# Performance work log

Measured on AMD Instinct MI355X. Metric: run time of the kernel, lower is better.

The kernel has to match this reference:

```python
import jax, jax.numpy as jnp
import numpy as np

D_MODEL = 1024
NUM_HEADS = 16
D_K = D_MODEL // NUM_HEADS
B, S = 2, 2048
NEG = -1e9


def setup_inputs() -> dict:
    key = jax.random.key(0)
    ks = jax.random.split(key, 12)
    scale = 1.0 / np.sqrt(D_MODEL)
    inp = {
        'q': jax.random.normal(ks[0], (B, S, D_MODEL), jnp.float32),
        'k': jax.random.normal(ks[1], (B, S, D_MODEL), jnp.float32),
        'v': jax.random.normal(ks[2], (B, S, D_MODEL), jnp.float32),
        'mask': jax.random.randint(ks[3], (1, 1, S, S), 0, 2, jnp.int32),
        'wq_w': jax.random.normal(ks[4], (D_MODEL, D_MODEL), jnp.float32) * scale,
        'wq_b': jnp.zeros((D_MODEL,), jnp.float32),
        'wk_w': jax.random.normal(ks[5], (D_MODEL, D_MODEL), jnp.float32) * scale,
        'wk_b': jnp.zeros((D_MODEL,), jnp.float32),
        'wv_w': jax.random.normal(ks[6], (D_MODEL, D_MODEL), jnp.float32) * scale,
        'wv_b': jnp.zeros((D_MODEL,), jnp.float32),
        'wo_w': jax.random.normal(ks[7], (D_MODEL, D_MODEL), jnp.float32) * scale,
        'wo_b': jnp.zeros((D_MODEL,), jnp.float32),
    }
    return inp


def _split_heads(x):
    # [B,S,D] -> [B,H,S,d_k]
    b, s, _ = x.shape
    return x.reshape(b, s, NUM_HEADS, D_K).transpose(0, 2, 1, 3)


def reference(q, k, v, mask, wq_w, wq_b, wk_w, wk_b, wv_w, wv_b, wo_w, wo_b):
    # torch Linear: y = x @ W.T + b
    qh = _split_heads(q @ wq_w.T + wq_b)
    kh = _split_heads(k @ wk_w.T + wk_b)
    vh = _split_heads(v @ wv_w.T + wv_b)
    scores = jnp.einsum('bhqd,bhkd->bhqk', qh, kh) / jnp.sqrt(jnp.float32(D_K))
    scores = jnp.where(mask == 0, jnp.float32(NEG), scores)
    attn = jax.nn.softmax(scores, axis=-1)  # dropout p=0 (eval): no-op
    x = jnp.einsum('bhqk,bhkd->bhqd', attn, vh)
    x = x.transpose(0, 2, 1, 3).reshape(q.shape[0], q.shape[1], D_MODEL)
    return x @ wo_w.T + wo_b
```

## Files before the change

### kernel.cpp

```cpp
#include <hip/hip_runtime.h>
#include <hip/hip_bf16.h>
#include <stdint.h>

#define S_LEN  2048
#define DMODEL 1024
#define NHEADS 16
#define DKH    64
#define KDIM   1024

typedef __bf16 bf16x8 __attribute__((ext_vector_type(8)));
typedef __bf16 bf16x2 __attribute__((ext_vector_type(2)));
typedef float  floatx4 __attribute__((ext_vector_type(4)));
typedef float  floatx16 __attribute__((ext_vector_type(16)));
typedef unsigned short ushort8v __attribute__((ext_vector_type(8)));
typedef unsigned int  uint32x2 __attribute__((ext_vector_type(2)));
typedef unsigned int  uint32x4 __attribute__((ext_vector_type(4)));

__device__ inline void gll16(const __bf16* g, const __bf16* l) {
    __builtin_amdgcn_global_load_lds(
        (const __attribute__((address_space(1))) void*)g,
        (__attribute__((address_space(3))) void*)l, 16, 0, 0);
}

__device__ inline float fast_exp2(float x) {
#if __has_builtin(__builtin_amdgcn_exp2f)
    return __builtin_amdgcn_exp2f(x);
#else
    return exp2f(x);
#endif
}

__device__ inline int bit_sign(uint32_t v, int idx) {
#if __has_builtin(__builtin_amdgcn_sbfe)
    return __builtin_amdgcn_sbfe((int)v, (uint32_t)idx, 1u);
#else
    return ((int)(v << (31 - idx))) >> 31;
#endif
}

__device__ inline void plswap(uint32_t& a, uint32_t& b) {
    asm volatile("v_permlane32_swap_b32 %0, %1" : "+v"(a), "+v"(b));
}

__global__ __launch_bounds__(256) void prep_kernel(
    const float* __restrict__ q, const float* __restrict__ k, const float* __restrict__ v,
    const float* __restrict__ wq, const float* __restrict__ wk, const float* __restrict__ wv,
    const float* __restrict__ wo, __bf16* __restrict__ out,
    const int* __restrict__ M, uint64_t* __restrict__ P) {
    if (blockIdx.x < 8192) {
        const size_t i8 = ((size_t)blockIdx.x * 256 + threadIdx.x) * 8;
        const float* src;
        if (i8 < 4194304u)        src = q  + i8;
        else if (i8 < 8388608u)   src = k  + (i8 - 4194304u);
        else if (i8 < 12582912u)  src = v  + (i8 - 8388608u);
        else if (i8 < 13631488u)  src = wq + (i8 - 12582912u);
        else if (i8 < 14680064u)  src = wk + (i8 - 13631488u);
        else if (i8 < 15728640u)  src = wv + (i8 - 14680064u);
        else                      src = wo + (i8 - 15728640u);
        floatx4 a = *(const floatx4*)src;
        floatx4 b = *(const floatx4*)(src + 4);
        bf16x8 r;
#pragma unroll
        for (int i = 0; i < 4; ++i) { r[i] = (__bf16)a[i]; r[i + 4] = (__bf16)b[i]; }
        *(bf16x8*)(out + i8) = r;
    } else {
        const size_t i = ((size_t)(blockIdx.x - 8192)) * 256 + threadIdx.x;
        uint64_t bits = __ballot(M[i] != 0);
        if ((threadIdx.x & 63) == 0) P[i >> 6] = bits;
    }
}

__global__ __launch_bounds__(256, 5) void qkv_gemm(
    const __bf16* __restrict__ qb, const __bf16* __restrict__ kb, const __bf16* __restrict__ vb,
    const __bf16* __restrict__ wqw, const __bf16* __restrict__ wkw, const __bf16* __restrict__ wvw,
    const float* __restrict__ biasq, const float* __restrict__ biask, const float* __restrict__ biasv,
    __bf16* __restrict__ qh, __bf16* __restrict__ kh, __bf16* __restrict__ vt) {
    __shared__ __align__(16) __bf16 As[2 * 128 * 32];
    __shared__ __align__(16) __bf16 Bs[2 * 64 * 32];

    const int lane = threadIdx.x & 63;
    const int wave = threadIdx.x >> 6;
    const int quad = lane >> 4;
    const int l15  = lane & 15;

    const int bid = blockIdx.x;
    const int job = bid >> 9;
    const int tt  = bid & 511;
    const __bf16* A; const __bf16* Bm; const float* bias; __bf16* C;
    int bx, by, MODE;
    if (job == 0)      { A = qb;  Bm = wqw; bias = biasq; C = qh; bx = tt & 15; by = tt >> 4; MODE = 0; }
    else if (job == 1) { A = kb;  Bm = wkw; bias = biask; C = kh; bx = tt & 15; by = tt >> 4; MODE = 0; }
    else               { A = wvw; Bm = vb;  bias = biasv; C = vt; bx = tt & 63; by = tt >> 6; MODE = 1; }

    const int m_t = by * 128, n_t = bx * 64;
    const int m0w = (wave >> 1) * 64, n0w = (wave & 1) * 32;

    const int lrow = lane >> 2;
    const int scol = ((lane & 3) ^ (lrow & 3)) * 8;

    floatx4 acc[4][2];
#pragma unroll
    for (int i = 0; i < 4; ++i)
#pragma unroll
        for (int j = 0; j < 2; ++j)
            acc[i][j] = (floatx4){0.f, 0.f, 0.f, 0.f};

    for (int kk = 0; kk < KDIM; kk += 64) {
#pragma unroll
        for (int u = 0; u < 6; ++u) {
            const int pi = wave * 6 + u;
            if (pi < 16) {
                const int panel = pi >> 3, rb = pi & 7;
                gll16(A + (size_t)(m_t + rb * 16 + lrow) * KDIM + kk + panel * 32 + scol,
                      As + (panel * 128 + rb * 16) * 32);
            } else {
                const int qi = pi - 16, panel = qi >> 2, rb = qi & 3;
                gll16(Bm + (size_t)(n_t + rb * 16 + lrow) * KDIM + kk + panel * 32 + scol,
                      Bs + (panel * 64 + rb * 16) * 32);
            }
        }
        __syncthreads();
        const int cq = (quad ^ (l15 & 3)) * 8;
#pragma unroll
        for (int p = 0; p < 2; ++p) {
            bf16x8 af[4], bfr[2];
#pragma unroll
            for (int i = 0; i < 4; ++i)
                af[i] = *(const bf16x8*)(As + (p * 128 + m0w + i * 16 + l15) * 32 + cq);
#pragma unroll
            for (int j = 0; j < 2; ++j)
                bfr[j] = *(const bf16x8*)(Bs + (p * 64 + n0w + j * 16 + l15) * 32 + cq);
#pragma unroll
            for (int i = 0; i < 4; ++i)
#pragma unroll
                for (int j = 0; j < 2; ++j)
                    acc[i][j] = __builtin_amdgcn_mfma_f32_16x16x32_bf16(af[i], bfr[j], acc[i][j], 0, 0, 0);
        }
        __syncthreads();
    }

#pragma unroll
    for (int j = 0; j < 2; ++j) {
        const int n = n_t + n0w + j * 16 + l15;
        float bn = (MODE == 1) ? 0.f : bias[n];
#pragma unroll
        for (int i = 0; i < 4; ++i) {
#pragma unroll
            for (int r = 0; r < 4; ++r) {
                const int m = m_t + m0w + i * 16 + quad * 4 + r;
                float bv = (MODE == 1) ? bias[m] : bn;
                float v = acc[i][j][r] + bv;
                size_t off;
                if (MODE == 0) {
                    off = ((size_t)((m >> 11) * 16 + (n >> 6)) * 2048 + (m & 2047)) * 64 + (n & 63);
                } else {
                    off = ((size_t)((n >> 11) * 16 + (m >> 6)) * 64 + (m & 63)) * 2048 + (n & 2047);
                }
                C[off] = (__bf16)v;
            }
        }
    }
}

__global__ __launch_bounds__(256) void gemm_out(const __bf16* __restrict__ A,
                                                const __bf16* __restrict__ Bm,
                                                const float* __restrict__ bias,
                                                float* __restrict__ C) {
    __shared__ __align__(16) __bf16 As[2 * 128 * 32];
    __shared__ __align__(16) __bf16 Bs[2 * 64 * 32];

    const int lane = threadIdx.x & 63;
    const int wave = threadIdx.x >> 6;
    const int quad = lane >> 4;
    const int l15  = lane & 15;
    const int m_t = blockIdx.y * 128, n_t = blockIdx.x * 64;
    const int m0w = (wave >> 1) * 64, n0w = (wave & 1) * 32;

    const int lrow = lane >> 2;
    const int scol = ((lane & 3) ^ (lrow & 3)) * 8;

    floatx4 acc[4][2];
#pragma unroll
    for (int i = 0; i < 4; ++i)
#pragma unroll
        for (int j = 0; j < 2; ++j)
            acc[i][j] = (floatx4){0.f, 0.f, 0.f, 0.f};

    for (int kk = 0; kk < KDIM; kk += 64) {
#pragma unroll
        for (int u = 0; u < 6; ++u) {
            const int pi = wave * 6 + u;
            if (pi < 16) {
                const int panel = pi >> 3, rb = pi & 7;
                gll16(A + (size_t)(m_t + rb * 16 + lrow) * KDIM + kk + panel * 32 + scol,
                      As + (panel * 128 + rb * 16) * 32);
            } else {
                const int qi = pi - 16, panel = qi >> 2, rb = qi & 3;
                gll16(Bm + (size_t)(n_t + rb * 16 + lrow) * KDIM + kk + panel * 32 + scol,
                      Bs + (panel * 64 + rb * 16) * 32);
            }
        }
        __syncthreads();
        const int cq = (quad ^ (l15 & 3)) * 8;
#pragma unroll
        for (int p = 0; p < 2; ++p) {
            bf16x8 af[4], bfr[2];
#pragma unroll
            for (int i = 0; i < 4; ++i)
                af[i] = *(const bf16x8*)(As + (p * 128 + m0w + i * 16 + l15) * 32 + cq);
#pragma unroll
            for (int j = 0; j < 2; ++j)
                bfr[j] = *(const bf16x8*)(Bs + (p * 64 + n0w + j * 16 + l15) * 32 + cq);
#pragma unroll
            for (int i = 0; i < 4; ++i)
#pragma unroll
                for (int j = 0; j < 2; ++j)
                    acc[i][j] = __builtin_amdgcn_mfma_f32_16x16x32_bf16(af[i], bfr[j], acc[i][j], 0, 0, 0);
        }
        __syncthreads();
    }

#pragma unroll
    for (int j = 0; j < 2; ++j) {
        const int n = n_t + n0w + j * 16 + l15;
        const float bn = bias[n];
#pragma unroll
        for (int i = 0; i < 4; ++i)
#pragma unroll
            for (int r = 0; r < 4; ++r) {
                const int m = m_t + m0w + i * 16 + quad * 4 + r;
                C[(size_t)m * 1024 + n] = acc[i][j][r] + bn;
            }
    }
}

__global__ __launch_bounds__(256, 4) void attn_kernel(const __bf16* __restrict__ Qh,
                                                      const __bf16* __restrict__ Kh,
                                                      const __bf16* __restrict__ Vt,
                                                      const uint64_t* __restrict__ PM,
                                                      __bf16* __restrict__ X) {
    __shared__ __align__(16) __bf16 Ks[2][4096];
    __shared__ __align__(16) __bf16 Vs[2][4096];

    const int lane = threadIdx.x & 63;
    const int wave = threadIdx.x >> 6;
    const int l31  = lane & 31;
    const int hi   = lane >> 5;
    const int kh   = wave & 1;
    const int qhf  = wave >> 1;

    const int bid  = blockIdx.x;
    const int xcd  = bid & 7;
    const int slot = bid >> 3;
    const int grp  = xcd * 4 + (slot >> 5);
    const int qt   = slot & 31;
    const int b = grp >> 4, h = grp & 15;
    const int qw = qt * 64 + qhf * 32;

    const __bf16* Qb = Qh + (size_t)(b * NHEADS + h) * S_LEN * DKH;
    const __bf16* Kb = Kh + (size_t)(b * NHEADS + h) * S_LEN * DKH;
    const __bf16* Vb = Vt + (size_t)(b * NHEADS + h) * DKH * S_LEN;
    const uint64_t* pr = PM + (size_t)(qw + l31) * (S_LEN / 64);

    const float cs = 0.18033688011112042f;

    uint32_t offK[2], offV[2];
#pragma unroll
    for (int i = 0; i < 2; ++i) {
        const int pi  = wave * 2 + i;
        const int khs = pi >> 2, kss = pi & 3;
        offK[i] = (uint32_t)((khs * 32 + l31) * DKH + kss * 16 + hi * 8);
        const int dts = pi >> 2, khv = (pi >> 1) & 1, cv = pi & 1;
        offV[i] = (uint32_t)((dts * 32 + l31) * S_LEN + khv * 32 + cv * 16 + hi * 8);
    }

    auto stage = [&](int p, int key0) {
#pragma unroll
        for (int i = 0; i < 2; ++i) {
            gll16(Kb + (size_t)key0 * DKH + offK[i], Ks[p] + (wave * 2 + i) * 512);
            gll16(Vb + (size_t)key0 + offV[i],       Vs[p] + (wave * 2 + i) * 512);
        }
    };

    bf16x8 qf[4];
#pragma unroll
    for (int ks = 0; ks < 4; ++ks)
        qf[ks] = *(const bf16x8*)(Qb + (size_t)(qw + l31) * DKH + ks * 16 + hi * 8);

    floatx16 o0, o1;
#pragma unroll
    for (int i = 0; i < 16; ++i) { o0[i] = 0.f; o1[i] = 0.f; }
    float ls0 = 0.f;

    const __bf16* Kl = &Ks[0][kh * 2048 + lane * 8];
    const __bf16* Vl = &Vs[0][kh * 1024 + lane * 8];

    stage(0, 0);
    uint64_t mwc = pr[0];

    for (int kt = 0; kt < 32; ++kt) {
        const int p = kt & 1;
        __syncthreads();
        if (kt < 31) stage(p ^ 1, (kt + 1) * 64);
        const uint64_t mw = mwc;
        if (kt < 31) mwc = pr[kt + 1];

        const __bf16* Kp = Kl + p * 4096;
        const __bf16* Vp = Vl + p * 4096;

        floatx16 st;
#pragma unroll
        for (int i = 0; i < 16; ++i) st[i] = 0.f;
#pragma unroll
        for (int ks = 0; ks < 4; ++ks) {
            bf16x8 kf = *(const bf16x8*)(Kp + ks * 512);
            st = __builtin_amdgcn_mfma_f32_32x32x16_bf16(kf, qf[ks], st, 0, 0, 0);
        }

        const uint32_t w32 = (uint32_t)(kh ? (mw >> 32) : mw);
        const uint32_t wsh = w32 >> (hi * 4);

        float e[16];
#pragma unroll
        for (int r = 0; r < 16; ++r) {
            const int cpos = (r & 3) + 8 * (r >> 2);
            float v = fast_exp2(st[r] * cs);
            const int sgn = bit_sign(wsh, cpos);
            e[r] = __builtin_bit_cast(float, __builtin_bit_cast(int, v) & sgn);
        }
        ls0 += (((e[0] + e[1]) + (e[2] + e[3])) + ((e[4] + e[5]) + (e[6] + e[7])))
             + (((e[8] + e[9]) + (e[10] + e[11])) + ((e[12] + e[13]) + (e[14] + e[15])));

        uint32_t w[8];
#pragma unroll
        for (int r2 = 0; r2 < 8; ++r2) {
            bf16x2 pp; pp[0] = (__bf16)e[2 * r2]; pp[1] = (__bf16)e[2 * r2 + 1];
            w[r2] = __builtin_bit_cast(uint32_t, pp);
        }
        plswap(w[0], w[2]);
        plswap(w[1], w[3]);
        plswap(w[4], w[6]);
        plswap(w[5], w[7]);
        uint32x4 f0 = {w[0], w[1], w[2], w[3]};
        uint32x4 f1 = {w[4], w[5], w[6], w[7]};
        bf16x8 pf0 = __builtin_bit_cast(bf16x8, f0);
        bf16x8 pf1 = __builtin_bit_cast(bf16x8, f1);

        bf16x8 vf;
        vf = *(const bf16x8*)(Vp + 0 * 2048 + 0 * 512);
        o0 = __builtin_amdgcn_mfma_f32_32x32x16_bf16(vf, pf0, o0, 0, 0, 0);
        vf = *(const bf16x8*)(Vp + 0 * 2048 + 1 * 512);
        o0 = __builtin_amdgcn_mfma_f32_32x32x16_bf16(vf, pf1, o0, 0, 0, 0);
        vf = *(const bf16x8*)(Vp + 1 * 2048 + 0 * 512);
        o1 = __builtin_amdgcn_mfma_f32_32x32x16_bf16(vf, pf0, o1, 0, 0, 0);
        vf = *(const bf16x8*)(Vp + 1 * 2048 + 1 * 512);
        o1 = __builtin_amdgcn_mfma_f32_32x32x16_bf16(vf, pf1, o1, 0, 0, 0);
    }

    float lsum2 = ls0 + __shfl_xor(ls0, 32);

    __syncthreads();
    float* red  = (float*)&Ks[0][0];
    float* redl = (float*)&Vs[0][0];
    if (kh == 1) {
#pragma unroll
        for (int g = 0; g < 16; ++g) red[(qhf * 32 + g) * 64 + lane] = o0[g];
#pragma unroll
        for (int g = 0; g < 16; ++g) red[(qhf * 32 + 16 + g) * 64 + lane] = o1[g];
        redl[qhf * 64 + lane] = lsum2;
    }
    __syncthreads();
    if (kh == 0) {
        const float lt  = lsum2 + redl[qhf * 64 + lane];
        const float inv = (lt > 0.f) ? (1.f / lt) : 0.f;
        unsigned short* xp = (unsigned short*)X +
            (size_t)(b * S_LEN + qw + l31) * DMODEL + h * DKH;
#pragma unroll
        for (int g = 0; g < 4; ++g) {
            float va = (o0[g * 4 + 0] + red[(qhf * 32 + g * 4 + 0) * 64 + lane]) * inv;
            float vb = (o0[g * 4 + 1] + red[(qhf * 32 + g * 4 + 1) * 64 + lane]) * inv;
            float vc = (o0[g * 4 + 2] + red[(qhf * 32 + g * 4 + 2) * 64 + lane]) * inv;
            float vd = (o0[g * 4 + 3] + red[(qhf * 32 + g * 4 + 3) * 64 + lane]) * inv;
            bf16x2 pa; pa[0] = (__bf16)va; pa[1] = (__bf16)vb;
            bf16x2 pb; pb[0] = (__bf16)vc; pb[1] = (__bf16)vd;
            uint32x2 wv = {__builtin_bit_cast(uint32_t, pa), __builtin_bit_cast(uint32_t, pb)};
            *(uint32x2*)(xp + g * 8 + hi * 4) = wv;
        }
#pragma unroll
        for (int g = 0; g < 4; ++g) {
            float va = (o1[g * 4 + 0] + red[(qhf * 32 + 16 + g * 4 + 0) * 64 + lane]) * inv;
            float vb = (o1[g * 4 + 1] + red[(qhf * 32 + 16 + g * 4 + 1) * 64 + lane]) * inv;
            float vc = (o1[g * 4 + 2] + red[(qhf * 32 + 16 + g * 4 + 2) * 64 + lane]) * inv;
            float vd = (o1[g * 4 + 3] + red[(qhf * 32 + 16 + g * 4 + 3) * 64 + lane]) * inv;
            bf16x2 pa; pa[0] = (__bf16)va; pa[1] = (__bf16)vb;
            bf16x2 pb; pb[0] = (__bf16)vc; pb[1] = (__bf16)vd;
            uint32x2 wv = {__builtin_bit_cast(uint32_t, pa), __builtin_bit_cast(uint32_t, pb)};
            *(uint32x2*)(xp + 32 + g * 8 + hi * 4) = wv;
        }
    }
}

extern "C" void kernel_launch(void* const* d_in, const int* in_sizes, int n_in,
                              void* d_out, int out_size, void* d_ws, size_t ws_size,
                              hipStream_t stream) {
    const float* q   = (const float*)d_in[0];
    const float* k   = (const float*)d_in[1];
    const float* v   = (const float*)d_in[2];
    const int*   msk = (const int*)d_in[3];
    const float* wq  = (const float*)d_in[4];
    const float* wqb = (const float*)d_in[5];
    const float* wk  = (const float*)d_in[6];
    const float* wkb = (const float*)d_in[7];
    const float* wv  = (const float*)d_in[8];
    const float* wvb = (const float*)d_in[9];
    const float* wo  = (const float*)d_in[10];
    const float* wob = (const float*)d_in[11];

    char* ws = (char*)d_ws;
    __bf16*   qh   = (__bf16*)(ws);
    __bf16*   kh   = (__bf16*)(ws + 8388608);
    __bf16*   vt   = (__bf16*)(ws + 16777216);
    uint64_t* pm   = (uint64_t*)(ws + 25165824);
    __bf16*   cb   = (__bf16*)(ws + 25690112);
    __bf16*   qb   = cb;
    __bf16*   kb   = cb + 4194304;
    __bf16*   vb   = cb + 8388608;
    __bf16*   wqbf = cb + 12582912;
    __bf16*   wkbf = cb + 13631488;
    __bf16*   wvbf = cb + 14680064;
    __bf16*   wobf = cb + 15728640;
    __bf16*   xa   = qb;

    prep_kernel<<<24576, 256, 0, stream>>>(q, k, v, wq, wk, wv, wo, cb, msk, pm);
    qkv_gemm<<<1536, 256, 0, stream>>>(qb, kb, vb, wqbf, wkbf, wvbf, wqb, wkb, wvb, qh, kh, vt);
    attn_kernel<<<1024, 256, 0, stream>>>(qh, kh, vt, pm, xa);
    gemm_out<<<dim3(16, 32), 256, 0, stream>>>(xa, wobf, wob, (float*)d_out);
}
```

Before: 285.8 us.

## Load K/V fragments directly from global to registers, drop LDS staging

Replaces the double-buffered LDS staging of K and V tiles with direct per-wave global loads into registers. K fragments are prefetched one tile ahead and the loop is unrolled by two. This removes the per-iteration block barrier and LDS traffic but exposes global load latency and raises register use. The permlane32 swap also uses the compiler builtin when available.

```diff
diff --git a/kernel.cpp b/kernel.cpp
--- a/kernel.cpp
+++ b/kernel.cpp
@@ -39,7 +39,13 @@
 }
 
 __device__ inline void plswap(uint32_t& a, uint32_t& b) {
+#if __has_builtin(__builtin_amdgcn_permlane32_swap)
+    auto r = __builtin_amdgcn_permlane32_swap((int)a, (int)b, false, false);
+    a = (uint32_t)r[0];
+    b = (uint32_t)r[1];
+#else
     asm volatile("v_permlane32_swap_b32 %0, %1" : "+v"(a), "+v"(b));
+#endif
 }
 
 __global__ __launch_bounds__(256) void prep_kernel(
@@ -239,8 +245,8 @@
                                                       const __bf16* __restrict__ Vt,
                                                       const uint64_t* __restrict__ PM,
                                                       __bf16* __restrict__ X) {
-    __shared__ __align__(16) __bf16 Ks[2][4096];
-    __shared__ __align__(16) __bf16 Vs[2][4096];
+    __shared__ __align__(16) float red[64 * 64];
+    __shared__ float redl[128];
 
     const int lane = threadIdx.x & 63;
     const int wave = threadIdx.x >> 6;
@@ -264,23 +270,9 @@
 
     const float cs = 0.18033688011112042f;
 
-    uint32_t offK[2], offV[2];
-#pragma unroll
-    for (int i = 0; i < 2; ++i) {
-        const int pi  = wave * 2 + i;
-        const int khs = pi >> 2, kss = pi & 3;
-        offK[i] = (uint32_t)((khs * 32 + l31) * DKH + kss * 16 + hi * 8);
-        const int dts = pi >> 2, khv = (pi >> 1) & 1, cv = pi & 1;
-        offV[i] = (uint32_t)((dts * 32 + l31) * S_LEN + khv * 32 + cv * 16 + hi * 8);
-    }
-
-    auto stage = [&](int p, int key0) {
-#pragma unroll
-        for (int i = 0; i < 2; ++i) {
-            gll16(Kb + (size_t)key0 * DKH + offK[i], Ks[p] + (wave * 2 + i) * 512);
-            gll16(Vb + (size_t)key0 + offV[i],       Vs[p] + (wave * 2 + i) * 512);
-        }
-    };
+    const int kOff  = l31 * DKH + hi * 8;
+    const int vOff0 = l31 * S_LEN + hi * 8;
+    const int vOff1 = (32 + l31) * S_LEN + hi * 8;
 
     bf16x8 qf[4];
 #pragma unroll
@@ -292,30 +284,44 @@
     for (int i = 0; i < 16; ++i) { o0[i] = 0.f; o1[i] = 0.f; }
     float ls0 = 0.f;
 
-    const __bf16* Kl = &Ks[0][kh * 2048 + lane * 8];
-    const __bf16* Vl = &Vs[0][kh * 1024 + lane * 8];
-
-    stage(0, 0);
+    bf16x8 kf0, kf1, kf2, kf3;
+    {
+        const __bf16* kp = Kb + (size_t)(kh * 32) * DKH + kOff;
+        kf0 = *(const bf16x8*)(kp);
+        kf1 = *(const bf16x8*)(kp + 16);
+        kf2 = *(const bf16x8*)(kp + 32);
+        kf3 = *(const bf16x8*)(kp + 48);
+    }
     uint64_t mwc = pr[0];
 
+#pragma unroll 2
     for (int kt = 0; kt < 32; ++kt) {
-        const int p = kt & 1;
-        __syncthreads();
-        if (kt < 31) stage(p ^ 1, (kt + 1) * 64);
+        const int kb0 = kt * 64 + kh * 32;
+
+        const __bf16* vp0 = Vb + (size_t)kb0 + vOff0;
+        const __bf16* vp1 = Vb + (size_t)kb0 + vOff1;
+        bf16x8 vf0 = *(const bf16x8*)(vp0);
+        bf16x8 vf1 = *(const bf16x8*)(vp0 + 16);
+        bf16x8 vf2 = *(const bf16x8*)(vp1);
+        bf16x8 vf3 = *(const bf16x8*)(vp1 + 16);
+
+        floatx16 st;
+#pragma unroll
+        for (int i = 0; i < 16; ++i) st[i] = 0.f;
+        st = __builtin_amdgcn_mfma_f32_32x32x16_bf16(kf0, qf[0], st, 0, 0, 0);
+        st = __builtin_amdgcn_mfma_f32_32x32x16_bf16(kf1, qf[1], st, 0, 0, 0);
+        st = __builtin_amdgcn_mfma_f32_32x32x16_bf16(kf2, qf[2], st, 0, 0, 0);
+        st = __builtin_amdgcn_mfma_f32_32x32x16_bf16(kf3, qf[3], st, 0, 0, 0);
+
+        if (kt < 31) {
+            const __bf16* kp = Kb + (size_t)(kb0 + 64) * DKH + kOff;
+            kf0 = *(const bf16x8*)(kp);
+            kf1 = *(const bf16x8*)(kp + 16);
+            kf2 = *(const bf16x8*)(kp + 32);
+            kf3 = *(const bf16x8*)(kp + 48);
+        }
         const uint64_t mw = mwc;
         if (kt < 31) mwc = pr[kt + 1];
-
-        const __bf16* Kp = Kl + p * 4096;
-        const __bf16* Vp = Vl + p * 4096;
-
-        floatx16 st;
-#pragma unroll
-        for (int i = 0; i < 16; ++i) st[i] = 0.f;
-#pragma unroll
-        for (int ks = 0; ks < 4; ++ks) {
-            bf16x8 kf = *(const bf16x8*)(Kp + ks * 512);
-            st = __builtin_amdgcn_mfma_f32_32x32x16_bf16(kf, qf[ks], st, 0, 0, 0);
-        }
 
         const uint32_t w32 = (uint32_t)(kh ? (mw >> 32) : mw);
         const uint32_t wsh = w32 >> (hi * 4);
@@ -346,22 +352,14 @@
         bf16x8 pf0 = __builtin_bit_cast(bf16x8, f0);
         bf16x8 pf1 = __builtin_bit_cast(bf16x8, f1);
 
-        bf16x8 vf;
-        vf = *(const bf16x8*)(Vp + 0 * 2048 + 0 * 512);
-        o0 = __builtin_amdgcn_mfma_f32_32x32x16_bf16(vf, pf0, o0, 0, 0, 0);
-        vf = *(const bf16x8*)(Vp + 0 * 2048 + 1 * 512);
-        o0 = __builtin_amdgcn_mfma_f32_32x32x16_bf16(vf, pf1, o0, 0, 0, 0);
-        vf = *(const bf16x8*)(Vp + 1 * 2048 + 0 * 512);
-        o1 = __builtin_amdgcn_mfma_f32_32x32x16_bf16(vf, pf0, o1, 0, 0, 0);
-        vf = *(const bf16x8*)(Vp + 1 * 2048 + 1 * 512);
-        o1 = __builtin_amdgcn_mfma_f32_32x32x16_bf16(vf, pf1, o1, 0, 0, 0);
+        o0 = __builtin_amdgcn_mfma_f32_32x32x16_bf16(vf0, pf0, o0, 0, 0, 0);
+        o0 = __builtin_amdgcn_mfma_f32_32x32x16_bf16(vf1, pf1, o0, 0, 0, 0);
+        o1 = __builtin_amdgcn_mfma_f32_32x32x16_bf16(vf2, pf0, o1, 0, 0, 0);
+        o1 = __builtin_amdgcn_mfma_f32_32x32x16_bf16(vf3, pf1, o1, 0, 0, 0);
     }
 
     float lsum2 = ls0 + __shfl_xor(ls0, 32);
 
-    __syncthreads();
-    float* red  = (float*)&Ks[0][0];
-    float* redl = (float*)&Vs[0][0];
     if (kh == 1) {
 #pragma unroll
         for (int g = 0; g < 16; ++g) red[(qhf * 32 + g) * 64 + lane] = o0[g];
```

Measured after the change: 388.0 us. 1.36x slower.
